# Performance work log

Measured on AMD Instinct MI355X. Metric: run time of the kernel, lower is better.

The kernel has to match this reference:

```python
import jax, jax.numpy as jnp
import numpy as np

N, B, H, L0, L1, C = 196608, 4096, 230, 10, 53, 53


def setup_inputs() -> dict:
    key = jax.random.key(0)
    ks = jax.random.split(key, 12)
    x = jax.random.normal(ks[0], (N, H), jnp.float32)
    label_index = jax.random.randint(ks[1], (N,), 0, C, dtype=jnp.int32)
    rl0 = jax.random.randint(ks[2], (C, 1), 0, L0, dtype=jnp.int32)
    rl1 = jax.random.randint(ks[3], (C, 1), 0, L1, dtype=jnp.int32)
    relation_levels = jnp.concatenate([rl0, rl1], axis=1)  # [C, 2]
    # equal-size bags: 4096 bags of 48 sentences (ragged boundaries)
    scope = (jnp.arange(B + 1, dtype=jnp.int32) * (N // B))
    rel_emb0 = jax.random.normal(ks[4], (L0, H), jnp.float32)
    rel_emb1 = jax.random.normal(ks[5], (L1, H), jnp.float32)
    att_w0 = jax.random.normal(ks[6], (L0,), jnp.float32)
    att_w1 = jax.random.normal(ks[7], (L1,), jnp.float32)
    w_s = jax.random.normal(ks[8], (2, 3 * H), jnp.float32) * 0.05
    b_s = jax.random.normal(ks[9], (2, 1), jnp.float32) * 0.05
    disc_matrix = jax.random.normal(ks[10], (C, 2 * H), jnp.float32) * 0.05
    bias = jnp.zeros((C,), jnp.float32)
    return {"x": x, "rel_emb0": rel_emb0, "rel_emb1": rel_emb1,
            "att_w0": att_w0, "att_w1": att_w1, "w_s": w_s, "b_s": b_s,
            "disc_matrix": disc_matrix, "bias": bias,
            "label_index": label_index, "relation_levels": relation_levels,
            "scope": scope}


def _segment_softmax(logits, seg, num_seg):
    # logits: [N]; stable softmax within each bag (segment)
    m = jax.ops.segment_max(logits, seg, num_segments=num_seg)
    e = jnp.exp(logits - m[seg])
    z = jax.ops.segment_sum(e, seg, num_segments=num_seg)
    return e / z[seg]


def reference(x, rel_emb0, rel_emb1, att_w0, att_w1, w_s, b_s, disc_matrix,
              bias, label_index, relation_levels, scope):
    n, h = x.shape
    num_bags = scope.shape[0] - 1
    # bag id of each sentence from ragged boundaries
    seg = jnp.searchsorted(scope, jnp.arange(n, dtype=scope.dtype), side="right") - 1

    ll = relation_levels[label_index]                 # [N, 2]
    r0 = rel_emb0[ll[:, 0]]                           # [N, H]
    r1 = rel_emb1[ll[:, 1]]                           # [N, H]
    s = jnp.tanh(jnp.concatenate([x, r0, r1], axis=-1))  # [N, 3H]
    logits = w_s @ s.T + b_s                          # [2, N]

    # per-bag ragged softmax over sentences, per hierarchy level
    score = jax.vmap(lambda l: _segment_softmax(l, seg, num_bags))(logits)  # [2, N]

    # vertical (hierarchy) attention: softmax over hier per sentence, mean per bag
    v = jnp.stack([att_w0[ll[:, 0]], att_w1[ll[:, 1]]])  # [2, N]
    vsm = jax.nn.softmax(v, axis=0)                      # [2, N]
    counts = jax.ops.segment_sum(jnp.ones((n,), x.dtype), seg, num_segments=num_bags)
    layer_att = jax.vmap(lambda r: jax.ops.segment_sum(r, seg, num_segments=num_bags))(vsm) / counts  # [2, B]

    # attention-weighted bag representation: per bag, [2, len] @ [len, H]
    rep = jax.vmap(lambda sc: jax.ops.segment_sum(sc[:, None] * x, seg, num_segments=num_bags))(score)  # [2, B, H]
    tower = (layer_att[:, :, None] * rep).transpose(1, 0, 2).reshape(num_bags, 2 * h)  # [B, 2H]

    return tower @ disc_matrix.T + bias  # [B, C]
```

## Files before the change

kernel.cpp:

```cpp
#include <hip/hip_runtime.h>

#define NTOT 196608
#define BAGS 4096
#define H 230
#define H3 690
#define NC 53

__device__ __forceinline__ float fast_tanh(float x) {
    float e = __expf(2.f * x);
    float r = __builtin_amdgcn_rcpf(e + 1.f);
    return fmaf(-2.f, r, 1.f);
}

__global__ void class_table_kernel(const float* __restrict__ rel_emb0,
                                   const float* __restrict__ rel_emb1,
                                   const float* __restrict__ att_w0,
                                   const float* __restrict__ att_w1,
                                   const float* __restrict__ w_s,
                                   const float* __restrict__ b_s,
                                   const int* __restrict__ relation_levels,
                                   float* __restrict__ cls)
{
    int c = blockIdx.x;
    int lane = threadIdx.x;
    int l0 = relation_levels[c * 2 + 0];
    int l1 = relation_levels[c * 2 + 1];
    float a00 = 0.f, a01 = 0.f, a10 = 0.f, a11 = 0.f;
    for (int j = lane; j < H; j += 64) {
        float t0 = fast_tanh(rel_emb0[l0 * H + j]);
        float t1 = fast_tanh(rel_emb1[l1 * H + j]);
        a00 += w_s[0 * H3 + H + j] * t0;
        a01 += w_s[0 * H3 + 2 * H + j] * t1;
        a10 += w_s[1 * H3 + H + j] * t0;
        a11 += w_s[1 * H3 + 2 * H + j] * t1;
    }
    for (int m = 32; m; m >>= 1) {
        a00 += __shfl_xor(a00, m);
        a01 += __shfl_xor(a01, m);
        a10 += __shfl_xor(a10, m);
        a11 += __shfl_xor(a11, m);
    }
    if (lane == 0) {
        cls[0 * NC + c] = a00 + a01 + b_s[0];
        cls[1 * NC + c] = a10 + a11 + b_s[1];
        float v0 = att_w0[l0], v1 = att_w1[l1];
        float mx = fmaxf(v0, v1);
        float e0 = __expf(v0 - mx), e1 = __expf(v1 - mx);
        float rz = __builtin_amdgcn_rcpf(e0 + e1);
        cls[2 * NC + c] = e0 * rz;
        cls[3 * NC + c] = e1 * rz;
    }
}

__global__ __launch_bounds__(256, 4) void bag_kernel(
    const float* __restrict__ x,
    const float* __restrict__ w_s,
    const float* __restrict__ disc,
    const float* __restrict__ bias,
    const int* __restrict__ label_index,
    const int* __restrict__ scope,
    const float* __restrict__ cls,
    float* __restrict__ out)
{
    __shared__ __align__(16) float part[4][464];
    __shared__ float zs[4][4];
    __shared__ __align__(16) float t01[464];

    int b = blockIdx.x;
    int start = scope[b];
    int cnt = scope[b + 1] - start;
    int tid = threadIdx.x;
    int wave = tid >> 6;
    int lane = tid & 63;
    const float* xb = x + (long long)start * H;

    const float2* w0p = (const float2*)w_s;
    const float2* w1p = (const float2*)(w_s + H3);
    float2 w0a = w0p[lane];
    float2 w1a = w1p[lane];
    float2 w0b = make_float2(0.f, 0.f), w1b = make_float2(0.f, 0.f);
    if (lane < 51) { w0b = w0p[64 + lane]; w1b = w1p[64 + lane]; }

    float2 acc0a = make_float2(0.f, 0.f), acc0b = make_float2(0.f, 0.f);
    float2 acc1a = make_float2(0.f, 0.f), acc1b = make_float2(0.f, 0.f);
    float z0 = 0.f, z1 = 0.f, sv0 = 0.f, sv1 = 0.f;

    if (cnt == 48) {
        int cl[12];
#pragma unroll
        for (int t = 0; t < 12; ++t)
            cl[t] = label_index[start + wave + 4 * t];

        float2 ra[12], rb[12];
#pragma unroll
        for (int t = 0; t < 12; ++t) {
            const float2* r2 = (const float2*)(xb + (wave + 4 * t) * H);
            ra[t] = r2[lane];
            rb[t] = (lane < 51) ? r2[64 + lane] : make_float2(0.f, 0.f);
        }

#pragma unroll
        for (int g = 0; g < 3; ++g) {
            float d0[4], d1[4];
#pragma unroll
            for (int k = 0; k < 4; ++k) {
                int t = 4 * g + k;
                float t0 = fast_tanh(ra[t].x), t1 = fast_tanh(ra[t].y);
                float t2 = fast_tanh(rb[t].x), t3 = fast_tanh(rb[t].y);
                d0[k] = w0a.x * t0 + w0a.y * t1 + w0b.x * t2 + w0b.y * t3;
                d1[k] = w1a.x * t0 + w1a.y * t1 + w1b.x * t2 + w1b.y * t3;
            }
#pragma unroll
            for (int m = 32; m; m >>= 1) {
#pragma unroll
                for (int k = 0; k < 4; ++k) {
                    d0[k] += __shfl_xor(d0[k], m);
                    d1[k] += __shfl_xor(d1[k], m);
                }
            }
#pragma unroll
            for (int k = 0; k < 4; ++k) {
                int t = 4 * g + k;
                int c = cl[t];
                float e0 = __expf(d0[k] + cls[c]);
                float e1 = __expf(d1[k] + cls[NC + c]);
                z0 += e0; z1 += e1;
                sv0 += cls[2 * NC + c];
                sv1 += cls[3 * NC + c];
                acc0a.x = fmaf(e0, ra[t].x, acc0a.x);
                acc0a.y = fmaf(e0, ra[t].y, acc0a.y);
                acc0b.x = fmaf(e0, rb[t].x, acc0b.x);
                acc0b.y = fmaf(e0, rb[t].y, acc0b.y);
                acc1a.x = fmaf(e1, ra[t].x, acc1a.x);
                acc1a.y = fmaf(e1, ra[t].y, acc1a.y);
                acc1b.x = fmaf(e1, rb[t].x, acc1b.x);
                acc1b.y = fmaf(e1, rb[t].y, acc1b.y);
            }
        }
    } else {
        for (int i = wave; i < cnt; i += 4) {
            const float2* r2 = (const float2*)(xb + (long long)i * H);
            float2 a = r2[lane];
            float2 bb = (lane < 51) ? r2[64 + lane] : make_float2(0.f, 0.f);
            float t0 = fast_tanh(a.x), t1 = fast_tanh(a.y);
            float t2 = fast_tanh(bb.x), t3 = fast_tanh(bb.y);
            float d0 = w0a.x * t0 + w0a.y * t1 + w0b.x * t2 + w0b.y * t3;
            float d1 = w1a.x * t0 + w1a.y * t1 + w1b.x * t2 + w1b.y * t3;
#pragma unroll
            for (int m = 32; m; m >>= 1) {
                d0 += __shfl_xor(d0, m);
                d1 += __shfl_xor(d1, m);
            }
            int c = label_index[start + i];
            float e0 = __expf(d0 + cls[c]);
            float e1 = __expf(d1 + cls[NC + c]);
            z0 += e0; z1 += e1;
            sv0 += cls[2 * NC + c];
            sv1 += cls[3 * NC + c];
            acc0a.x = fmaf(e0, a.x,  acc0a.x); acc0a.y = fmaf(e0, a.y,  acc0a.y);
            acc0b.x = fmaf(e0, bb.x, acc0b.x); acc0b.y = fmaf(e0, bb.y, acc0b.y);
            acc1a.x = fmaf(e1, a.x,  acc1a.x); acc1a.y = fmaf(e1, a.y,  acc1a.y);
            acc1b.x = fmaf(e1, bb.x, acc1b.x); acc1b.y = fmaf(e1, bb.y, acc1b.y);
        }
    }

    float2* pw = (float2*)part[wave];
    pw[lane]       = acc0a;
    pw[115 + lane] = acc1a;
    if (lane < 51) {
        pw[64 + lane]       = acc0b;
        pw[115 + 64 + lane] = acc1b;
    }
    if (lane == 0) {
        zs[wave][0] = z0; zs[wave][1] = z1;
        zs[wave][2] = sv0; zs[wave][3] = sv1;
    }
    __syncthreads();

    float zt0 = zs[0][0] + zs[1][0] + zs[2][0] + zs[3][0];
    float zt1 = zs[0][1] + zs[1][1] + zs[2][1] + zs[3][1];
    float st0 = zs[0][2] + zs[1][2] + zs[2][2] + zs[3][2];
    float st1 = zs[0][3] + zs[1][3] + zs[2][3] + zs[3][3];
    float rc  = __builtin_amdgcn_rcpf((float)cnt);
    float s0  = st0 * rc * __builtin_amdgcn_rcpf(zt0);
    float s1  = st1 * rc * __builtin_amdgcn_rcpf(zt1);

    for (int t = tid; t < 2 * H; t += 256) {
        float s = part[0][t] + part[1][t] + part[2][t] + part[3][t];
        t01[t] = s * (t < H ? s0 : s1);
    }
    __syncthreads();

    int q = tid & 3;
    int c = tid >> 2;
    if (c < NC) {
        const float4* drow4 = (const float4*)(disc + c * (2 * H));
        const float4* t4 = (const float4*)t01;
        float acc = 0.f;
        for (int k = q; k < 115; k += 4) {
            float4 dv = drow4[k];
            float4 tv = t4[k];
            acc += dv.x * tv.x + dv.y * tv.y + dv.z * tv.z + dv.w * tv.w;
        }
        acc += __shfl_down(acc, 2, 4);
        acc += __shfl_down(acc, 1, 4);
        if (q == 0) out[b * NC + c] = acc + bias[c];
    }
}

extern "C" void kernel_launch(void* const* d_in, const int* in_sizes, int n_in,
                              void* d_out, int out_size, void* d_ws, size_t ws_size,
                              hipStream_t stream) {
    const float* x               = (const float*)d_in[0];
    const float* rel_emb0        = (const float*)d_in[1];
    const float* rel_emb1        = (const float*)d_in[2];
    const float* att_w0          = (const float*)d_in[3];
    const float* att_w1          = (const float*)d_in[4];
    const float* w_s             = (const float*)d_in[5];
    const float* b_s             = (const float*)d_in[6];
    const float* disc            = (const float*)d_in[7];
    const float* bias            = (const float*)d_in[8];
    const int*   label_index     = (const int*)d_in[9];
    const int*   relation_levels = (const int*)d_in[10];
    const int*   scope           = (const int*)d_in[11];
    float* out = (float*)d_out;
    float* cls = (float*)d_ws;

    class_table_kernel<<<NC, 64, 0, stream>>>(rel_emb0, rel_emb1, att_w0, att_w1,
                                              w_s, b_s, relation_levels, cls);
    bag_kernel<<<BAGS, 256, 0, stream>>>(x, w_s, disc, bias, label_index, scope,
                                         cls, out);
}
```

Measured before the change: 303.3 us.

## Replace fully-unrolled 12-row register preload with double-buffered streaming loop

The 48-row fast path used to preload all 12 rows per wave into registers. It now streams them one at a time with a one-row-ahead prefetch, and launch bounds are raised to 8 blocks per CU. Uniform values such as the scope bounds, the wave index and the labels are moved to scalar registers with readfirstlane. The aim is to cut VGPR pressure so more waves are resident to hide memory latency. The cost is less memory-level parallelism per wave, since only one row is in flight instead of twelve, and pointer offsets now use int instead of long long.

```diff
diff --git a/kernel.cpp b/kernel.cpp
--- a/kernel.cpp
+++ b/kernel.cpp
@@ -52,7 +52,7 @@
     }
 }
 
-__global__ __launch_bounds__(256, 4) void bag_kernel(
+__global__ __launch_bounds__(256, 8) void bag_kernel(
     const float* __restrict__ x,
     const float* __restrict__ w_s,
     const float* __restrict__ disc,
@@ -67,12 +67,13 @@
     __shared__ __align__(16) float t01[464];
 
     int b = blockIdx.x;
-    int start = scope[b];
-    int cnt = scope[b + 1] - start;
     int tid = threadIdx.x;
     int wave = tid >> 6;
     int lane = tid & 63;
-    const float* xb = x + (long long)start * H;
+
+    int start = __builtin_amdgcn_readfirstlane(scope[b]);
+    int cnt   = __builtin_amdgcn_readfirstlane(scope[b + 1]) - start;
+    int swave = __builtin_amdgcn_readfirstlane(wave);
 
     const float2* w0p = (const float2*)w_s;
     const float2* w1p = (const float2*)(w_s + H3);
@@ -86,60 +87,65 @@
     float z0 = 0.f, z1 = 0.f, sv0 = 0.f, sv1 = 0.f;
 
     if (cnt == 48) {
-        int cl[12];
-#pragma unroll
-        for (int t = 0; t < 12; ++t)
-            cl[t] = label_index[start + wave + 4 * t];
-
-        float2 ra[12], rb[12];
-#pragma unroll
-        for (int t = 0; t < 12; ++t) {
-            const float2* r2 = (const float2*)(xb + (wave + 4 * t) * H);
-            ra[t] = r2[lane];
-            rb[t] = (lane < 51) ? r2[64 + lane] : make_float2(0.f, 0.f);
-        }
-
-#pragma unroll
-        for (int g = 0; g < 3; ++g) {
-            float d0[4], d1[4];
-#pragma unroll
-            for (int k = 0; k < 4; ++k) {
-                int t = 4 * g + k;
-                float t0 = fast_tanh(ra[t].x), t1 = fast_tanh(ra[t].y);
-                float t2 = fast_tanh(rb[t].x), t3 = fast_tanh(rb[t].y);
-                d0[k] = w0a.x * t0 + w0a.y * t1 + w0b.x * t2 + w0b.y * t3;
-                d1[k] = w1a.x * t0 + w1a.y * t1 + w1b.x * t2 + w1b.y * t3;
-            }
+        int roff0 = (start + swave) * H;
+        const float2* rp0 = (const float2*)(x + roff0);
+        float2 a  = rp0[lane];
+        float2 bb = (lane < 51) ? rp0[64 + lane] : make_float2(0.f, 0.f);
+        int c0 = __builtin_amdgcn_readfirstlane(label_index[start + swave]);
+        float k0 = cls[c0],        k1 = cls[NC + c0];
+        float p0 = cls[2*NC + c0], p1 = cls[3*NC + c0];
+
+#pragma unroll 1
+        for (int t = 0; t < 11; ++t) {
+            int roff = (start + swave + 4 * (t + 1)) * H;
+            const float2* rp = (const float2*)(x + roff);
+            float2 na  = rp[lane];
+            float2 nbb = (lane < 51) ? rp[64 + lane] : make_float2(0.f, 0.f);
+            int nc = __builtin_amdgcn_readfirstlane(
+                         label_index[start + swave + 4 * (t + 1)]);
+            float nk0 = cls[nc],        nk1 = cls[NC + nc];
+            float np0 = cls[2*NC + nc], np1 = cls[3*NC + nc];
+
+            float t0 = fast_tanh(a.x),  t1 = fast_tanh(a.y);
+            float t2 = fast_tanh(bb.x), t3 = fast_tanh(bb.y);
+            float d0 = w0a.x * t0 + w0a.y * t1 + w0b.x * t2 + w0b.y * t3;
+            float d1 = w1a.x * t0 + w1a.y * t1 + w1b.x * t2 + w1b.y * t3;
 #pragma unroll
             for (int m = 32; m; m >>= 1) {
+                d0 += __shfl_xor(d0, m);
+                d1 += __shfl_xor(d1, m);
+            }
+            float e0 = __expf(d0 + k0);
+            float e1 = __expf(d1 + k1);
+            z0 += e0; z1 += e1; sv0 += p0; sv1 += p1;
+            acc0a.x = fmaf(e0, a.x,  acc0a.x); acc0a.y = fmaf(e0, a.y,  acc0a.y);
+            acc0b.x = fmaf(e0, bb.x, acc0b.x); acc0b.y = fmaf(e0, bb.y, acc0b.y);
+            acc1a.x = fmaf(e1, a.x,  acc1a.x); acc1a.y = fmaf(e1, a.y,  acc1a.y);
+            acc1b.x = fmaf(e1, bb.x, acc1b.x); acc1b.y = fmaf(e1, bb.y, acc1b.y);
+
+            a = na; bb = nbb; k0 = nk0; k1 = nk1; p0 = np0; p1 = np1;
+        }
+        {
+            float t0 = fast_tanh(a.x),  t1 = fast_tanh(a.y);
+            float t2 = fast_tanh(bb.x), t3 = fast_tanh(bb.y);
+            float d0 = w0a.x * t0 + w0a.y * t1 + w0b.x * t2 + w0b.y * t3;
+            float d1 = w1a.x * t0 + w1a.y * t1 + w1b.x * t2 + w1b.y * t3;
 #pragma unroll
-                for (int k = 0; k < 4; ++k) {
-                    d0[k] += __shfl_xor(d0[k], m);
-                    d1[k] += __shfl_xor(d1[k], m);
-                }
+            for (int m = 32; m; m >>= 1) {
+                d0 += __shfl_xor(d0, m);
+                d1 += __shfl_xor(d1, m);
             }
-#pragma unroll
-            for (int k = 0; k < 4; ++k) {
-                int t = 4 * g + k;
-                int c = cl[t];
-                float e0 = __expf(d0[k] + cls[c]);
-                float e1 = __expf(d1[k] + cls[NC + c]);
-                z0 += e0; z1 += e1;
-                sv0 += cls[2 * NC + c];
-                sv1 += cls[3 * NC + c];
-                acc0a.x = fmaf(e0, ra[t].x, acc0a.x);
-                acc0a.y = fmaf(e0, ra[t].y, acc0a.y);
-                acc0b.x = fmaf(e0, rb[t].x, acc0b.x);
-                acc0b.y = fmaf(e0, rb[t].y, acc0b.y);
-                acc1a.x = fmaf(e1, ra[t].x, acc1a.x);
-                acc1a.y = fmaf(e1, ra[t].y, acc1a.y);
-                acc1b.x = fmaf(e1, rb[t].x, acc1b.x);
-                acc1b.y = fmaf(e1, rb[t].y, acc1b.y);
-            }
+            float e0 = __expf(d0 + k0);
+            float e1 = __expf(d1 + k1);
+            z0 += e0; z1 += e1; sv0 += p0; sv1 += p1;
+            acc0a.x = fmaf(e0, a.x,  acc0a.x); acc0a.y = fmaf(e0, a.y,  acc0a.y);
+            acc0b.x = fmaf(e0, bb.x, acc0b.x); acc0b.y = fmaf(e0, bb.y, acc0b.y);
+            acc1a.x = fmaf(e1, a.x,  acc1a.x); acc1a.y = fmaf(e1, a.y,  acc1a.y);
+            acc1b.x = fmaf(e1, bb.x, acc1b.x); acc1b.y = fmaf(e1, bb.y, acc1b.y);
         }
     } else {
-        for (int i = wave; i < cnt; i += 4) {
-            const float2* r2 = (const float2*)(xb + (long long)i * H);
+        for (int i = swave; i < cnt; i += 4) {
+            const float2* r2 = (const float2*)(x + (start + i) * H);
             float2 a = r2[lane];
             float2 bb = (lane < 51) ? r2[64 + lane] : make_float2(0.f, 0.f);
             float t0 = fast_tanh(a.x), t1 = fast_tanh(a.y);
@@ -151,7 +157,7 @@
                 d0 += __shfl_xor(d0, m);
                 d1 += __shfl_xor(d1, m);
             }
-            int c = label_index[start + i];
+            int c = __builtin_amdgcn_readfirstlane(label_index[start + i]);
             float e0 = __expf(d0 + cls[c]);
             float e1 = __expf(d1 + cls[NC + c]);
             z0 += e0; z1 += e1;
```

After: 298.9 us. Within noise of the previous version (-1.5%).
